# Kernel tuning notes

Measured on AMD Instinct MI355X. Metric: run time of the kernel, lower is better.

The kernel has to match this reference:

```python
import jax, jax.numpy as jnp
import numpy as np

B, N, E, H, R, L, VOCAB, KINDS = 8, 4096, 524288, 128, 8, 2, 100000, 8


def setup_inputs() -> dict:
    key = jax.random.key(0)
    ks = jax.random.split(key, 12)
    concept_ids = jax.random.randint(ks[0], (B, N), 1, VOCAB)  # avoid padding_idx 0
    kind_ids = jax.random.randint(ks[1], (B, N), 0, KINDS)
    node_mask = jnp.ones((B, N), dtype=jnp.int32)
    # edges constrained within each batch block (module assumes per-subgraph edges)
    e_batch = jax.random.randint(ks[2], (E,), 0, B)
    src = e_batch * N + jax.random.randint(ks[3], (E,), 0, N)
    dst = e_batch * N + jax.random.randint(ks[4], (E,), 0, N)
    edge_index = jnp.stack([src, dst], axis=0)
    edge_type = jax.random.randint(ks[5], (E,), 0, R)
    s = 0.02
    concept_emb = jax.random.normal(ks[6], (VOCAB, H), jnp.float32) * s
    concept_emb = concept_emb.at[0].set(0.0)  # padding_idx=0
    kind_emb = jax.random.normal(ks[7], (KINDS, H), jnp.float32) * s
    proj_W = jax.random.normal(ks[8], (H, H), jnp.float32) * s
    proj_b = jnp.zeros((H,), jnp.float32)
    self_W = jax.random.normal(ks[9], (L, H, H), jnp.float32) * s
    self_b = jnp.zeros((L, H), jnp.float32)
    rel_W = jax.random.normal(ks[10], (L, R, H, H), jnp.float32) * s
    return dict(pkg_node_concept_ids=concept_ids, pkg_node_kind_ids=kind_ids,
                pkg_node_mask=node_mask, pkg_edge_index=edge_index,
                pkg_edge_type=edge_type, concept_emb=concept_emb, kind_emb=kind_emb,
                proj_W=proj_W, proj_b=proj_b, self_W=self_W, self_b=self_b, rel_W=rel_W)


def reference(pkg_node_concept_ids, pkg_node_kind_ids, pkg_node_mask,
              pkg_edge_index, pkg_edge_type, concept_emb, kind_emb,
              proj_W, proj_b, self_W, self_b, rel_W):
    b, n = pkg_node_concept_ids.shape
    num_nodes = b * n
    # input embedding + projection (dropout = identity in eval)
    x = concept_emb[pkg_node_concept_ids] + kind_emb[pkg_node_kind_ids]  # [B,N,H]
    x = jnp.einsum('bnh,gh->bng', x, proj_W) + proj_b
    x = x.reshape(num_nodes, -1)  # packed node states [B*N, H]
    src, dst = pkg_edge_index[0], pkg_edge_index[1]
    deg = jax.ops.segment_sum(jnp.ones_like(src, dtype=x.dtype), dst,
                              num_segments=num_nodes)[:, None]
    deg = jnp.maximum(deg, 1.0)
    n_layers, n_rel = rel_W.shape[0], rel_W.shape[1]
    for l in range(n_layers):
        xs = x[src]  # [E,H] gather
        msgs = jnp.zeros_like(xs)
        for r in range(n_rel):
            msgs = msgs + jnp.where((pkg_edge_type == r)[:, None],
                                    xs @ rel_W[l, r].T, 0.0)
        agg = jax.ops.segment_sum(msgs, dst, num_segments=num_nodes) / deg
        x = jax.nn.relu(x @ self_W[l].T + self_b[l] + agg)
    out = x.reshape(b, n, -1) * pkg_node_mask[..., None].astype(x.dtype)
    return out
```

## Files before the change

kernel.cpp:

```cpp
#include <hip/hip_runtime.h>
#include <hip/hip_bf16.h>

#define NODES 32768
#define HD 128
#define NE 524288
#define NR 8

typedef unsigned int u32;
typedef unsigned short u16;
typedef __attribute__((ext_vector_type(8))) short bf16x8;
typedef __attribute__((ext_vector_type(4))) float f32x4;

#define XH_OFF   (0u)
#define XL_OFF   (8u<<20)
#define Y_OFF    (16u<<20)
#define Z_OFF    (80u<<20)
#define ADJ_OFF  (96u<<20)
#define RP_OFF   (98u<<20)
#define CUR_OFF  ((98u<<20)+(256u<<10))
#define BSUM_OFF ((98u<<20)+(512u<<10))
#define BP_OFF   ((98u<<20)+(640u<<10))

#define BP_LAYER 294912

__device__ __forceinline__ float bflo(u32 u){ union{u32 i;float f;}c; c.i=u<<16; return c.f; }
__device__ __forceinline__ float bfhi(u32 u){ union{u32 i;float f;}c; c.i=u&0xffff0000u; return c.f; }
__device__ __forceinline__ u16 f2bf(float f){
  u32 u=__float_as_uint(f);
  u32 r=u + 0x7fffu + ((u>>16)&1u);
  return (u16)(r>>16);
}
__device__ __forceinline__ float bf2f(u16 h){ return __uint_as_float(((u32)h)<<16); }

__device__ __forceinline__ void gl_lds16(const void* g, void* l){
  __builtin_amdgcn_global_load_lds((const __attribute__((address_space(1))) u32*)g,
                                   (__attribute__((address_space(3))) u32*)l, 16, 0, 0);
}

__device__ __forceinline__ void fma64(const float* At, const float* Wt,
                                      int mq, int gq, float acc[8][4])
{
#pragma unroll 8
  for(int kk=0;kk<64;kk++){
    const float4 a0=*(const float4*)&At[kk*68+mq*8];
    const float4 a1=*(const float4*)&At[kk*68+mq*8+4];
    const float4 w =*(const float4*)&Wt[kk*132+gq*4];
    float av[8]={a0.x,a0.y,a0.z,a0.w,a1.x,a1.y,a1.z,a1.w};
#pragma unroll
    for(int i=0;i<8;i++){
      acc[i][0]=fmaf(av[i],w.x,acc[i][0]);
      acc[i][1]=fmaf(av[i],w.y,acc[i][1]);
      acc[i][2]=fmaf(av[i],w.z,acc[i][2]);
      acc[i][3]=fmaf(av[i],w.w,acc[i][3]);
    }
  }
}

__global__ __launch_bounds__(256) void embed_gemm(
    const int* __restrict__ cid, const int* __restrict__ kid,
    const float* __restrict__ cemb, const float* __restrict__ kemb,
    const float* __restrict__ pW, const float* __restrict__ pb,
    u16* __restrict__ xh, u16* __restrict__ xl)
{
  __shared__ float At[64*68];
  __shared__ float Wt[64*132];
  const int tid=threadIdx.x;
  const int d0=blockIdx.x*64;
  const int mq=tid>>5, gq=tid&31;
  float acc[8][4];
#pragma unroll
  for(int i=0;i<8;i++){ acc[i][0]=0.f; acc[i][1]=0.f; acc[i][2]=0.f; acc[i][3]=0.f; }

  for(int c=0;c<2;c++){
    const int h0=c*64;
    __syncthreads();
    { int m=tid>>2; int hh=(tid&3)*16;
      int ci=cid[d0+m], ki=kid[d0+m];
      const float* cp=cemb+(size_t)ci*HD+h0+hh;
      const float* kp=kemb+(size_t)ki*HD+h0+hh;
      float* ap=&At[hh*68+m];
#pragma unroll
      for(int j=0;j<16;j+=4){
        float4 a=*(const float4*)(cp+j);
        float4 b=*(const float4*)(kp+j);
        ap[(j+0)*68]=a.x+b.x; ap[(j+1)*68]=a.y+b.y;
        ap[(j+2)*68]=a.z+b.z; ap[(j+3)*68]=a.w+b.w;
      }
    }
    { int g=tid>>1; int hh=(tid&1)*32;
      const float* wp=pW+(size_t)g*HD+h0+hh;
      float* wl=&Wt[hh*132+g];
#pragma unroll
      for(int j=0;j<32;j+=4){
        float4 w=*(const float4*)(wp+j);
        wl[(j+0)*132]=w.x; wl[(j+1)*132]=w.y; wl[(j+2)*132]=w.z; wl[(j+3)*132]=w.w;
      }
    }
    __syncthreads();
    fma64(At,Wt,mq,gq,acc);
  }
  const float4 bias=*(const float4*)&pb[gq*4];
#pragma unroll
  for(int i=0;i<8;i++){
    int m=d0+mq*8+i;
    float v[4]={acc[i][0]+bias.x,acc[i][1]+bias.y,acc[i][2]+bias.z,acc[i][3]+bias.w};
    u16 hb[4], lb[4];
#pragma unroll
    for(int j=0;j<4;j++){ hb[j]=f2bf(v[j]); lb[j]=f2bf(v[j]-bf2f(hb[j])); }
    uint2 hv={(u32)hb[0]|((u32)hb[1]<<16),(u32)hb[2]|((u32)hb[3]<<16)};
    uint2 lv={(u32)lb[0]|((u32)lb[1]<<16),(u32)lb[2]|((u32)lb[3]<<16)};
    *(uint2*)&xh[(size_t)m*HD+gq*4]=hv;
    *(uint2*)&xl[(size_t)m*HD+gq*4]=lv;
  }
}

__global__ void prep_w(const float* __restrict__ rW, const float* __restrict__ sW,
                       u16* __restrict__ Bp)
{
  int idx=blockIdx.x*256+threadIdx.x;
  int l=idx/147456;
  int rem=idx%147456;
  int t=rem>>14;
  int kn=rem&16383;
  int k=kn>>7, n=kn&127;
  float w;
  if(t<8) w=rW[(((size_t)l*NR+t)*HD+n)*HD+k];
  else    w=sW[((size_t)l*HD+n)*HD+k];
  u16* base=Bp+(size_t)l*BP_LAYER+(size_t)t*32768;
  int ks=k>>5, q=(k>>3)&3, j=k&7;
  size_t off=((size_t)ks*128+n)*32+q*8+j;
  u16 hb=f2bf(w);
  u16 lb=f2bf(w-bf2f(hb));
  base[off]=hb;
  base[off+16384]=lb;
}

__global__ void count_deg(const int* __restrict__ dst, u32* __restrict__ cnt){
  int e=blockIdx.x*256+threadIdx.x;
  atomicAdd(&cnt[dst[e]],1u);
}

__global__ void scan1(const u32* __restrict__ cnt, u32* __restrict__ rp, u32* __restrict__ bsum){
  __shared__ u32 sh[256];
  int t=threadIdx.x; int base=blockIdx.x*256;
  u32 v=cnt[base+t]; sh[t]=v; __syncthreads();
  for(int off=1;off<256;off<<=1){
    u32 tv=(t>=off)?sh[t-off]:0u; __syncthreads();
    sh[t]+=tv; __syncthreads();
  }
  rp[base+t]=sh[t]-v;
  if(t==255) bsum[blockIdx.x]=sh[255];
}

__global__ void scan2(u32* __restrict__ bsum, u32* __restrict__ rp){
  __shared__ u32 sh[128];
  int t=threadIdx.x;
  u32 v=bsum[t]; sh[t]=v; __syncthreads();
  for(int off=1;off<128;off<<=1){
    u32 tv=(t>=off)?sh[t-off]:0u; __syncthreads();
    sh[t]+=tv; __syncthreads();
  }
  bsum[t]=sh[t]-v;
  if(t==0) rp[NODES]=NE;
}

__global__ void scan3(u32* __restrict__ rp, const u32* __restrict__ bsum){
  int i=blockIdx.x*256+threadIdx.x;
  rp[i]+=bsum[blockIdx.x];
}

__global__ void scatter_edges(const int* __restrict__ src, const int* __restrict__ dst,
                              const int* __restrict__ et, const u32* __restrict__ rp,
                              u32* __restrict__ cur, u32* __restrict__ adj){
  int e=blockIdx.x*256+threadIdx.x;
  int d=dst[e];
  u32 pos=atomicAdd(&cur[d],1u);
  adj[rp[d]+pos]=(u32)src[e] | ((u32)et[e]<<16);
}

__global__ __launch_bounds__(256,3) void gemm_y(
    const u16* __restrict__ xhi, const u16* __restrict__ xlo,
    const u16* __restrict__ Bt, u16* __restrict__ y, float* __restrict__ z)
{
  __shared__ u16 Atile[128*128];
  const int tid=threadIdx.x;
  const int wave=tid>>6, lane=tid&63;
  const int wm=wave>>1, wn=wave&1;
  const int q=lane>>4;
  const int d0=blockIdx.x*128;
  const int t=blockIdx.y;
  const u16* Btile=Bt+(size_t)t*32768;

  f32x4 acc[4][4];
#pragma unroll
  for(int a=0;a<4;a++)
#pragma unroll
    for(int b=0;b<4;b++) acc[a][b]=(f32x4){0.f,0.f,0.f,0.f};

  const int st_c  = lane&15;
  const int st_rin= lane>>4;

#pragma unroll
  for(int i=0;i<8;i++){
    int rbase=wave*32+i*4;
    int r=rbase+st_rin;
    int g=st_c ^ (r&15);
    gl_lds16(xhi+(size_t)(d0+r)*HD+g*8, &Atile[rbase*128]);
  }
  __syncthreads();

#pragma unroll
  for(int ks=0;ks<4;ks++){
    bf16x8 afr[4];
#pragma unroll
    for(int tm=0;tm<4;tm++){
      int m=wm*64+tm*16+(lane&15);
      afr[tm]=*(const bf16x8*)&Atile[m*128+(((ks*4)+q)^(m&15))*8];
    }
#pragma unroll
    for(int s=0;s<2;s++){
      const u16* Bb=Btile+s*16384;
#pragma unroll
      for(int tn=0;tn<4;tn++){
        int n=wn*64+tn*16+(lane&15);
        bf16x8 bfr=*(const bf16x8*)&Bb[((size_t)ks*128+n)*32+q*8];
#pragma unroll
        for(int tm=0;tm<4;tm++)
          acc[tm][tn]=__builtin_amdgcn_mfma_f32_16x16x32_bf16(afr[tm],bfr,acc[tm][tn],0,0,0);
      }
    }
  }

  __syncthreads();
#pragma unroll
  for(int i=0;i<8;i++){
    int rbase=wave*32+i*4;
    int r=rbase+st_rin;
    int g=st_c ^ (r&15);
    gl_lds16(xlo+(size_t)(d0+r)*HD+g*8, &Atile[rbase*128]);
  }
  __syncthreads();

#pragma unroll
  for(int ks=0;ks<4;ks++){
    bf16x8 afr[4];
#pragma unroll
    for(int tm=0;tm<4;tm++){
      int m=wm*64+tm*16+(lane&15);
      afr[tm]=*(const bf16x8*)&Atile[m*128+(((ks*4)+q)^(m&15))*8];
    }
#pragma unroll
    for(int tn=0;tn<4;tn++){
      int n=wn*64+tn*16+(lane&15);
      bf16x8 bfr=*(const bf16x8*)&Btile[((size_t)ks*128+n)*32+q*8];
#pragma unroll
      for(int tm=0;tm<4;tm++)
        acc[tm][tn]=__builtin_amdgcn_mfma_f32_16x16x32_bf16(afr[tm],bfr,acc[tm][tn],0,0,0);
    }
  }

  if(t<8){
    u16* yt=y+((size_t)t*NODES+d0)*HD;
#pragma unroll
    for(int tn=0;tn<4;tn++){
      int n=wn*64+tn*16+(lane&15);
#pragma unroll
      for(int tm=0;tm<4;tm++){
        int rbase=wm*64+tm*16+q*4;
#pragma unroll
        for(int r=0;r<4;r++)
          yt[(size_t)(rbase+r)*HD+n]=f2bf(acc[tm][tn][r]);
      }
    }
  } else {
    float* zt=z+(size_t)d0*HD;
#pragma unroll
    for(int tn=0;tn<4;tn++){
      int n=wn*64+tn*16+(lane&15);
#pragma unroll
      for(int tm=0;tm<4;tm++){
        int rbase=wm*64+tm*16+q*4;
#pragma unroll
        for(int r=0;r<4;r++)
          zt[(size_t)(rbase+r)*HD+n]=acc[tm][tn][r];
      }
    }
  }
}

__global__ __launch_bounds__(256) void gather_combine(
    const u32* __restrict__ y, const float* __restrict__ z,
    const u32* __restrict__ adj, const u32* __restrict__ rp,
    const float* __restrict__ sb, const int* __restrict__ mask,
    u32* __restrict__ xh, u32* __restrict__ xl, float* __restrict__ outf, int last)
{
  const int wave=threadIdx.x>>6, lane=threadIdx.x&63;
  const int node=blockIdx.x*4+wave;
  const int beg=(int)rp[node], end=(int)rp[node+1];
  float a0=0.f, a1=0.f;
  int e=beg;
  for(; e+8<=end; e+=8){
    u32 qv[8], vv[8];
#pragma unroll
    for(int i=0;i<8;i++) qv[i]=adj[e+i];
#pragma unroll
    for(int i=0;i<8;i++) vv[i]=y[((size_t)(qv[i]>>16)*NODES+(qv[i]&0x7fffu))*64+lane];
#pragma unroll
    for(int i=0;i<8;i++){ a0+=bflo(vv[i]); a1+=bfhi(vv[i]); }
  }
  for(; e<end; ++e){
    u32 qq=adj[e];
    u32 v=y[((size_t)(qq>>16)*NODES+(qq&0x7fffu))*64+lane];
    a0+=bflo(v); a1+=bfhi(v);
  }
  float inv=1.f/fmaxf((float)(end-beg),1.f);
  float2 zz=*(const float2*)&z[(size_t)node*HD+2*lane];
  float2 bb=*(const float2*)&sb[2*lane];
  float v0=fmaxf(zz.x+a0*inv+bb.x,0.f);
  float v1=fmaxf(zz.y+a1*inv+bb.y,0.f);
  if(last){
    float mk=(float)mask[node];
    float2 o={v0*mk,v1*mk};
    *(float2*)&outf[(size_t)node*HD+2*lane]=o;
  } else {
    u16 h0=f2bf(v0), h1=f2bf(v1);
    u16 l0=f2bf(v0-bf2f(h0)), l1=f2bf(v1-bf2f(h1));
    xh[(size_t)node*64+lane]=(u32)h0|((u32)h1<<16);
    xl[(size_t)node*64+lane]=(u32)l0|((u32)l1<<16);
  }
}

extern "C" void kernel_launch(void* const* d_in, const int* in_sizes, int n_in,
                              void* d_out, int out_size, void* d_ws, size_t ws_size,
                              hipStream_t stream)
{
  (void)in_sizes; (void)n_in; (void)out_size; (void)ws_size;
  const int*   cid =(const int*)  d_in[0];
  const int*   kid =(const int*)  d_in[1];
  const int*   mask=(const int*)  d_in[2];
  const int*   ei  =(const int*)  d_in[3];
  const int*   et  =(const int*)  d_in[4];
  const float* cemb=(const float*)d_in[5];
  const float* kemb=(const float*)d_in[6];
  const float* pW  =(const float*)d_in[7];
  const float* pb  =(const float*)d_in[8];
  const float* sW  =(const float*)d_in[9];
  const float* sb  =(const float*)d_in[10];
  const float* rW  =(const float*)d_in[11];
  float* out=(float*)d_out;
  char*  ws =(char*)d_ws;

  u16* xh =(u16*)(ws+XH_OFF);
  u16* xl =(u16*)(ws+XL_OFF);
  u16* y  =(u16*)(ws+Y_OFF);
  float* z=(float*)(ws+Z_OFF);
  u32* adj =(u32*)(ws+ADJ_OFF);
  u32* rp  =(u32*)(ws+RP_OFF);
  u32* cur =(u32*)(ws+CUR_OFF);
  u32* bsum=(u32*)(ws+BSUM_OFF);
  u16* Bp  =(u16*)(ws+BP_OFF);
  const int* srcA=ei;
  const int* dstA=ei+NE;

  hipMemsetAsync(cur,0,NODES*sizeof(u32),stream);
  prep_w<<<1152,256,0,stream>>>(rW,sW,Bp);
  embed_gemm<<<NODES/64,256,0,stream>>>(cid,kid,cemb,kemb,pW,pb,xh,xl);
  count_deg<<<NE/256,256,0,stream>>>(dstA,cur);
  scan1<<<NODES/256,256,0,stream>>>(cur,rp,bsum);
  scan2<<<1,128,0,stream>>>(bsum,rp);
  scan3<<<NODES/256,256,0,stream>>>(rp,bsum);
  hipMemsetAsync(cur,0,NODES*sizeof(u32),stream);
  scatter_edges<<<NE/256,256,0,stream>>>(srcA,dstA,et,rp,cur,adj);

  gemm_y<<<dim3(NODES/128,9),256,0,stream>>>(xh,xl,Bp,y,z);
  gather_combine<<<NODES/4,256,0,stream>>>((const u32*)y,z,adj,rp,sb,mask,(u32*)xh,(u32*)xl,out,0);
  gemm_y<<<dim3(NODES/128,9),256,0,stream>>>(xh,xl,Bp+BP_LAYER,y,z);
  gather_combine<<<NODES/4,256,0,stream>>>((const u32*)y,z,adj,rp,sb+HD,mask,(u32*)xh,(u32*)xl,out,1);
}
```

Measured before the change: 343.1 us.

## Use MFMA for embedding projection, fold scan fixup, restructure gather and GEMM

Several changes land together. The FP32 FMA embedding projection becomes a split-bf16 MFMA GEMM, with the projection weight prepacked in prep_w. The scan3 kernel and the second memset go away by folding the block offsets into the consumers and clearing the counter inside scan1. gemm_y loads the hi and lo tiles together into a doubled LDS buffer at 2 blocks per CU. gather_combine now loads 64 adjacency entries per wave, broadcasts them with shuffles, and gathers two edges per wave with 8-byte loads, using a precomputed flat row index. The risks are lower occupancy in gemm_y and extra adds in the gather.

Result: faster. 312.2 us (-9.0%).

```diff
diff --git a/kernel.cpp b/kernel.cpp
--- a/kernel.cpp
+++ b/kernel.cpp
@@ -22,6 +22,7 @@
 #define BP_OFF   ((98u<<20)+(640u<<10))
 
 #define BP_LAYER 294912
+#define PP_ELEM  589824
 
 __device__ __forceinline__ float bflo(u32 u){ union{u32 i;float f;}c; c.i=u<<16; return c.f; }
 __device__ __forceinline__ float bfhi(u32 u){ union{u32 i;float f;}c; c.i=u&0xffff0000u; return c.f; }
@@ -37,102 +38,142 @@
                                    (__attribute__((address_space(3))) u32*)l, 16, 0, 0);
 }
 
-__device__ __forceinline__ void fma64(const float* At, const float* Wt,
-                                      int mq, int gq, float acc[8][4])
+__global__ void prep_w(const float* __restrict__ rW, const float* __restrict__ sW,
+                       const float* __restrict__ pWg, u16* __restrict__ Bp)
 {
-#pragma unroll 8
-  for(int kk=0;kk<64;kk++){
-    const float4 a0=*(const float4*)&At[kk*68+mq*8];
-    const float4 a1=*(const float4*)&At[kk*68+mq*8+4];
-    const float4 w =*(const float4*)&Wt[kk*132+gq*4];
-    float av[8]={a0.x,a0.y,a0.z,a0.w,a1.x,a1.y,a1.z,a1.w};
-#pragma unroll
-    for(int i=0;i<8;i++){
-      acc[i][0]=fmaf(av[i],w.x,acc[i][0]);
-      acc[i][1]=fmaf(av[i],w.y,acc[i][1]);
-      acc[i][2]=fmaf(av[i],w.z,acc[i][2]);
-      acc[i][3]=fmaf(av[i],w.w,acc[i][3]);
-    }
-  }
-}
-
-__global__ __launch_bounds__(256) void embed_gemm(
+  int idx=blockIdx.x*256+threadIdx.x;
+  if(idx<294912){
+    int l=idx/147456;
+    int rem=idx%147456;
+    int t=rem>>14;
+    int kn=rem&16383;
+    int k=kn>>7, n=kn&127;
+    float w;
+    if(t<8) w=rW[(((size_t)l*NR+t)*HD+n)*HD+k];
+    else    w=sW[((size_t)l*HD+n)*HD+k];
+    u16* base=Bp+(size_t)l*BP_LAYER+(size_t)t*32768;
+    int ks=k>>5, q=(k>>3)&3, j=k&7;
+    size_t off=((size_t)ks*128+n)*32+q*8+j;
+    u16 hb=f2bf(w);
+    u16 lb=f2bf(w-bf2f(hb));
+    base[off]=hb;
+    base[off+16384]=lb;
+  } else {
+    int kn=idx-294912;
+    int k=kn>>7, n=kn&127;
+    float w=pWg[(size_t)n*HD+k];
+    u16* base=Bp+PP_ELEM;
+    int ks=k>>5, q=(k>>3)&3, j=k&7;
+    size_t off=((size_t)ks*128+n)*32+q*8+j;
+    u16 hb=f2bf(w);
+    u16 lb=f2bf(w-bf2f(hb));
+    base[off]=hb;
+    base[off+16384]=lb;
+  }
+}
+
+__global__ __launch_bounds__(256,2) void embed_mfma(
     const int* __restrict__ cid, const int* __restrict__ kid,
     const float* __restrict__ cemb, const float* __restrict__ kemb,
-    const float* __restrict__ pW, const float* __restrict__ pb,
+    const u16* __restrict__ PP, const float* __restrict__ pb,
     u16* __restrict__ xh, u16* __restrict__ xl)
 {
-  __shared__ float At[64*68];
-  __shared__ float Wt[64*132];
+  __shared__ u16 Atile[2][128*128];
   const int tid=threadIdx.x;
-  const int d0=blockIdx.x*64;
-  const int mq=tid>>5, gq=tid&31;
-  float acc[8][4];
-#pragma unroll
-  for(int i=0;i<8;i++){ acc[i][0]=0.f; acc[i][1]=0.f; acc[i][2]=0.f; acc[i][3]=0.f; }
-
-  for(int c=0;c<2;c++){
-    const int h0=c*64;
-    __syncthreads();
-    { int m=tid>>2; int hh=(tid&3)*16;
-      int ci=cid[d0+m], ki=kid[d0+m];
-      const float* cp=cemb+(size_t)ci*HD+h0+hh;
-      const float* kp=kemb+(size_t)ki*HD+h0+hh;
-      float* ap=&At[hh*68+m];
-#pragma unroll
-      for(int j=0;j<16;j+=4){
-        float4 a=*(const float4*)(cp+j);
-        float4 b=*(const float4*)(kp+j);
-        ap[(j+0)*68]=a.x+b.x; ap[(j+1)*68]=a.y+b.y;
-        ap[(j+2)*68]=a.z+b.z; ap[(j+3)*68]=a.w+b.w;
-      }
-    }
-    { int g=tid>>1; int hh=(tid&1)*32;
-      const float* wp=pW+(size_t)g*HD+h0+hh;
-      float* wl=&Wt[hh*132+g];
-#pragma unroll
-      for(int j=0;j<32;j+=4){
-        float4 w=*(const float4*)(wp+j);
-        wl[(j+0)*132]=w.x; wl[(j+1)*132]=w.y; wl[(j+2)*132]=w.z; wl[(j+3)*132]=w.w;
-      }
-    }
-    __syncthreads();
-    fma64(At,Wt,mq,gq,acc);
-  }
-  const float4 bias=*(const float4*)&pb[gq*4];
-#pragma unroll
-  for(int i=0;i<8;i++){
-    int m=d0+mq*8+i;
-    float v[4]={acc[i][0]+bias.x,acc[i][1]+bias.y,acc[i][2]+bias.z,acc[i][3]+bias.w};
-    u16 hb[4], lb[4];
-#pragma unroll
-    for(int j=0;j<4;j++){ hb[j]=f2bf(v[j]); lb[j]=f2bf(v[j]-bf2f(hb[j])); }
-    uint2 hv={(u32)hb[0]|((u32)hb[1]<<16),(u32)hb[2]|((u32)hb[3]<<16)};
-    uint2 lv={(u32)lb[0]|((u32)lb[1]<<16),(u32)lb[2]|((u32)lb[3]<<16)};
-    *(uint2*)&xh[(size_t)m*HD+gq*4]=hv;
-    *(uint2*)&xl[(size_t)m*HD+gq*4]=lv;
-  }
-}
-
-__global__ void prep_w(const float* __restrict__ rW, const float* __restrict__ sW,
-                       u16* __restrict__ Bp)
-{
-  int idx=blockIdx.x*256+threadIdx.x;
-  int l=idx/147456;
-  int rem=idx%147456;
-  int t=rem>>14;
-  int kn=rem&16383;
-  int k=kn>>7, n=kn&127;
-  float w;
-  if(t<8) w=rW[(((size_t)l*NR+t)*HD+n)*HD+k];
-  else    w=sW[((size_t)l*HD+n)*HD+k];
-  u16* base=Bp+(size_t)l*BP_LAYER+(size_t)t*32768;
-  int ks=k>>5, q=(k>>3)&3, j=k&7;
-  size_t off=((size_t)ks*128+n)*32+q*8+j;
-  u16 hb=f2bf(w);
-  u16 lb=f2bf(w-bf2f(hb));
-  base[off]=hb;
-  base[off+16384]=lb;
+  const int wave=tid>>6, lane=tid&63;
+  const int wm=wave>>1, wn=wave&1;
+  const int q=lane>>4;
+  const int d0=blockIdx.x*128;
+
+  { int r=tid>>1, half=tid&1;
+    int ci=cid[d0+r], ki=kid[d0+r];
+    const float* cp=cemb+(size_t)ci*HD+half*64;
+    const float* kp=kemb+(size_t)ki*HD+half*64;
+#pragma unroll
+    for(int cc=0;cc<8;cc++){
+      float4 a0=*(const float4*)(cp+cc*8);
+      float4 a1=*(const float4*)(cp+cc*8+4);
+      float4 b0=*(const float4*)(kp+cc*8);
+      float4 b1=*(const float4*)(kp+cc*8+4);
+      float v[8]={a0.x+b0.x,a0.y+b0.y,a0.z+b0.z,a0.w+b0.w,
+                  a1.x+b1.x,a1.y+b1.y,a1.z+b1.z,a1.w+b1.w};
+      u16 hb[8], lb[8];
+#pragma unroll
+      for(int j=0;j<8;j++){ hb[j]=f2bf(v[j]); lb[j]=f2bf(v[j]-bf2f(hb[j])); }
+      int chunk=half*8+cc;
+      int dst=r*128+(chunk^(r&15))*8;
+      uint4 hv={(u32)hb[0]|((u32)hb[1]<<16),(u32)hb[2]|((u32)hb[3]<<16),
+                (u32)hb[4]|((u32)hb[5]<<16),(u32)hb[6]|((u32)hb[7]<<16)};
+      uint4 lv={(u32)lb[0]|((u32)lb[1]<<16),(u32)lb[2]|((u32)lb[3]<<16),
+                (u32)lb[4]|((u32)lb[5]<<16),(u32)lb[6]|((u32)lb[7]<<16)};
+      *(uint4*)&Atile[0][dst]=hv;
+      *(uint4*)&Atile[1][dst]=lv;
+    }
+  }
+  __syncthreads();
+
+  f32x4 acc[4][4];
+#pragma unroll
+  for(int a=0;a<4;a++)
+#pragma unroll
+    for(int b=0;b<4;b++) acc[a][b]=(f32x4){0.f,0.f,0.f,0.f};
+
+#pragma unroll
+  for(int ks=0;ks<4;ks++){
+    bf16x8 ah[4];
+#pragma unroll
+    for(int tm=0;tm<4;tm++){
+      int m=wm*64+tm*16+(lane&15);
+      ah[tm]=*(const bf16x8*)&Atile[0][m*128+(((ks*4)+q)^(m&15))*8];
+    }
+#pragma unroll
+    for(int s=0;s<2;s++){
+      const u16* Bb=PP+s*16384;
+#pragma unroll
+      for(int tn=0;tn<4;tn++){
+        int n=wn*64+tn*16+(lane&15);
+        bf16x8 bfr=*(const bf16x8*)&Bb[((size_t)ks*128+n)*32+q*8];
+#pragma unroll
+        for(int tm=0;tm<4;tm++)
+          acc[tm][tn]=__builtin_amdgcn_mfma_f32_16x16x32_bf16(ah[tm],bfr,acc[tm][tn],0,0,0);
+      }
+    }
+  }
+#pragma unroll
+  for(int ks=0;ks<4;ks++){
+    bf16x8 al[4];
+#pragma unroll
+    for(int tm=0;tm<4;tm++){
+      int m=wm*64+tm*16+(lane&15);
+      al[tm]=*(const bf16x8*)&Atile[1][m*128+(((ks*4)+q)^(m&15))*8];
+    }
+#pragma unroll
+    for(int tn=0;tn<4;tn++){
+      int n=wn*64+tn*16+(lane&15);
+      bf16x8 bfr=*(const bf16x8*)&PP[((size_t)ks*128+n)*32+q*8];
+#pragma unroll
+      for(int tm=0;tm<4;tm++)
+        acc[tm][tn]=__builtin_amdgcn_mfma_f32_16x16x32_bf16(al[tm],bfr,acc[tm][tn],0,0,0);
+    }
+  }
+
+#pragma unroll
+  for(int tn=0;tn<4;tn++){
+    int n=wn*64+tn*16+(lane&15);
+    float b=pb[n];
+#pragma unroll
+    for(int tm=0;tm<4;tm++){
+      int rbase=d0+wm*64+tm*16+q*4;
+#pragma unroll
+      for(int r=0;r<4;r++){
+        float v=acc[tm][tn][r]+b;
+        u16 hb=f2bf(v);
+        u16 lb=f2bf(v-bf2f(hb));
+        xh[(size_t)(rbase+r)*HD+n]=hb;
+        xl[(size_t)(rbase+r)*HD+n]=lb;
+      }
+    }
+  }
 }
 
 __global__ void count_deg(const int* __restrict__ dst, u32* __restrict__ cnt){
@@ -140,10 +181,12 @@
   atomicAdd(&cnt[dst[e]],1u);
 }
 
-__global__ void scan1(const u32* __restrict__ cnt, u32* __restrict__ rp, u32* __restrict__ bsum){
+__global__ void scan1(u32* __restrict__ cnt, u32* __restrict__ rp, u32* __restrict__ bsum){
   __shared__ u32 sh[256];
   int t=threadIdx.x; int base=blockIdx.x*256;
-  u32 v=cnt[base+t]; sh[t]=v; __syncthreads();
+  u32 v=cnt[base+t]; sh[t]=v;
+  cnt[base+t]=0u;
+  __syncthreads();
   for(int off=1;off<256;off<<=1){
     u32 tv=(t>=off)?sh[t-off]:0u; __syncthreads();
     sh[t]+=tv; __syncthreads();
@@ -161,28 +204,24 @@
     sh[t]+=tv; __syncthreads();
   }
   bsum[t]=sh[t]-v;
-  if(t==0) rp[NODES]=NE;
-}
-
-__global__ void scan3(u32* __restrict__ rp, const u32* __restrict__ bsum){
-  int i=blockIdx.x*256+threadIdx.x;
-  rp[i]+=bsum[blockIdx.x];
+  if(t==0){ rp[NODES]=NE; bsum[128]=0u; }
 }
 
 __global__ void scatter_edges(const int* __restrict__ src, const int* __restrict__ dst,
                               const int* __restrict__ et, const u32* __restrict__ rp,
+                              const u32* __restrict__ bsum,
                               u32* __restrict__ cur, u32* __restrict__ adj){
   int e=blockIdx.x*256+threadIdx.x;
   int d=dst[e];
   u32 pos=atomicAdd(&cur[d],1u);
-  adj[rp[d]+pos]=(u32)src[e] | ((u32)et[e]<<16);
-}
-
-__global__ __launch_bounds__(256,3) void gemm_y(
+  adj[rp[d]+bsum[d>>8]+pos]=(u32)(et[e]*NODES+src[e]);
+}
+
+__global__ __launch_bounds__(256,2) void gemm_y(
     const u16* __restrict__ xhi, const u16* __restrict__ xlo,
     const u16* __restrict__ Bt, u16* __restrict__ y, float* __restrict__ z)
 {
-  __shared__ u16 Atile[128*128];
+  __shared__ u16 Atile[2][128*128];
   const int tid=threadIdx.x;
   const int wave=tid>>6, lane=tid&63;
   const int wm=wave>>1, wn=wave&1;
@@ -191,12 +230,6 @@
   const int t=blockIdx.y;
   const u16* Btile=Bt+(size_t)t*32768;
 
-  f32x4 acc[4][4];
-#pragma unroll
-  for(int a=0;a<4;a++)
-#pragma unroll
-    for(int b=0;b<4;b++) acc[a][b]=(f32x4){0.f,0.f,0.f,0.f};
-
   const int st_c  = lane&15;
   const int st_rin= lane>>4;
 
@@ -205,49 +238,51 @@
     int rbase=wave*32+i*4;
     int r=rbase+st_rin;
     int g=st_c ^ (r&15);
-    gl_lds16(xhi+(size_t)(d0+r)*HD+g*8, &Atile[rbase*128]);
-  }
-  __syncthreads();
-
-#pragma unroll
-  for(int ks=0;ks<4;ks++){
-    bf16x8 afr[4];
-#pragma unroll
-    for(int tm=0;tm<4;tm++){
-      int m=wm*64+tm*16+(lane&15);
-      afr[tm]=*(const bf16x8*)&Atile[m*128+(((ks*4)+q)^(m&15))*8];
-    }
-#pragma unroll
-    for(int s=0;s<2;s++){
-      const u16* Bb=Btile+s*16384;
-#pragma unroll
-      for(int tn=0;tn<4;tn++){
-        int n=wn*64+tn*16+(lane&15);
-        bf16x8 bfr=*(const bf16x8*)&Bb[((size_t)ks*128+n)*32+q*8];
-#pragma unroll
-        for(int tm=0;tm<4;tm++)
-          acc[tm][tn]=__builtin_amdgcn_mfma_f32_16x16x32_bf16(afr[tm],bfr,acc[tm][tn],0,0,0);
-      }
-    }
-  }
-
-  __syncthreads();
+    gl_lds16(xhi+(size_t)(d0+r)*HD+g*8, &Atile[0][rbase*128]);
+  }
 #pragma unroll
   for(int i=0;i<8;i++){
     int rbase=wave*32+i*4;
     int r=rbase+st_rin;
     int g=st_c ^ (r&15);
-    gl_lds16(xlo+(size_t)(d0+r)*HD+g*8, &Atile[rbase*128]);
+    gl_lds16(xlo+(size_t)(d0+r)*HD+g*8, &Atile[1][rbase*128]);
   }
   __syncthreads();
 
+  f32x4 acc[4][4];
+#pragma unroll
+  for(int a=0;a<4;a++)
+#pragma unroll
+    for(int b=0;b<4;b++) acc[a][b]=(f32x4){0.f,0.f,0.f,0.f};
+
 #pragma unroll
   for(int ks=0;ks<4;ks++){
-    bf16x8 afr[4];
+    bf16x8 ah[4];
 #pragma unroll
     for(int tm=0;tm<4;tm++){
       int m=wm*64+tm*16+(lane&15);
-      afr[tm]=*(const bf16x8*)&Atile[m*128+(((ks*4)+q)^(m&15))*8];
+      ah[tm]=*(const bf16x8*)&Atile[0][m*128+(((ks*4)+q)^(m&15))*8];
+    }
+#pragma unroll
+    for(int s=0;s<2;s++){
+      const u16* Bb=Btile+s*16384;
+#pragma unroll
+      for(int tn=0;tn<4;tn++){
+        int n=wn*64+tn*16+(lane&15);
+        bf16x8 bfr=*(const bf16x8*)&Bb[((size_t)ks*128+n)*32+q*8];
+#pragma unroll
+        for(int tm=0;tm<4;tm++)
+          acc[tm][tn]=__builtin_amdgcn_mfma_f32_16x16x32_bf16(ah[tm],bfr,acc[tm][tn],0,0,0);
+      }
+    }
+  }
+#pragma unroll
+  for(int ks=0;ks<4;ks++){
+    bf16x8 al[4];
+#pragma unroll
+    for(int tm=0;tm<4;tm++){
+      int m=wm*64+tm*16+(lane&15);
+      al[tm]=*(const bf16x8*)&Atile[1][m*128+(((ks*4)+q)^(m&15))*8];
     }
 #pragma unroll
     for(int tn=0;tn<4;tn++){
@@ -255,7 +290,7 @@
       bf16x8 bfr=*(const bf16x8*)&Btile[((size_t)ks*128+n)*32+q*8];
 #pragma unroll
       for(int tm=0;tm<4;tm++)
-        acc[tm][tn]=__builtin_amdgcn_mfma_f32_16x16x32_bf16(afr[tm],bfr,acc[tm][tn],0,0,0);
+        acc[tm][tn]=__builtin_amdgcn_mfma_f32_16x16x32_bf16(al[tm],bfr,acc[tm][tn],0,0,0);
     }
   }
 
@@ -289,44 +324,73 @@
 }
 
 __global__ __launch_bounds__(256) void gather_combine(
-    const u32* __restrict__ y, const float* __restrict__ z,
-    const u32* __restrict__ adj, const u32* __restrict__ rp,
+    const uint2* __restrict__ yy, const float* __restrict__ z,
+    const u32* __restrict__ adj, const u32* __restrict__ rp, const u32* __restrict__ bsum,
     const float* __restrict__ sb, const int* __restrict__ mask,
     u32* __restrict__ xh, u32* __restrict__ xl, float* __restrict__ outf, int last)
 {
   const int wave=threadIdx.x>>6, lane=threadIdx.x&63;
   const int node=blockIdx.x*4+wave;
-  const int beg=(int)rp[node], end=(int)rp[node+1];
-  float a0=0.f, a1=0.f;
-  int e=beg;
-  for(; e+8<=end; e+=8){
-    u32 qv[8], vv[8];
-#pragma unroll
-    for(int i=0;i<8;i++) qv[i]=adj[e+i];
-#pragma unroll
-    for(int i=0;i<8;i++) vv[i]=y[((size_t)(qv[i]>>16)*NODES+(qv[i]&0x7fffu))*64+lane];
-#pragma unroll
-    for(int i=0;i<8;i++){ a0+=bflo(vv[i]); a1+=bfhi(vv[i]); }
-  }
-  for(; e<end; ++e){
-    u32 qq=adj[e];
-    u32 v=y[((size_t)(qq>>16)*NODES+(qq&0x7fffu))*64+lane];
-    a0+=bflo(v); a1+=bfhi(v);
-  }
-  float inv=1.f/fmaxf((float)(end-beg),1.f);
-  float2 zz=*(const float2*)&z[(size_t)node*HD+2*lane];
-  float2 bb=*(const float2*)&sb[2*lane];
-  float v0=fmaxf(zz.x+a0*inv+bb.x,0.f);
-  float v1=fmaxf(zz.y+a1*inv+bb.y,0.f);
-  if(last){
-    float mk=(float)mask[node];
-    float2 o={v0*mk,v1*mk};
-    *(float2*)&outf[(size_t)node*HD+2*lane]=o;
-  } else {
-    u16 h0=f2bf(v0), h1=f2bf(v1);
-    u16 l0=f2bf(v0-bf2f(h0)), l1=f2bf(v1-bf2f(h1));
-    xh[(size_t)node*64+lane]=(u32)h0|((u32)h1<<16);
-    xl[(size_t)node*64+lane]=(u32)l0|((u32)l1<<16);
+  const int sub=lane>>5, c=lane&31;
+  const int beg=(int)(rp[node]+bsum[node>>8]);
+  const int end=(int)(rp[node+1]+bsum[(node+1)>>8]);
+  float a0=0.f,a1=0.f,a2=0.f,a3=0.f;
+
+  for(int base=beg; base<end; base+=64){
+    int nk=end-base; if(nk>64) nk=64;
+    u32 adjv = (lane<nk) ? adj[base+lane] : 0u;
+    int i=0;
+    for(; i+16<=nk; i+=16){
+      uint2 vv[8];
+#pragma unroll
+      for(int j=0;j<8;j++){
+        u32 row=(u32)__shfl((int)adjv, i+j*2+sub);
+        vv[j]=yy[(size_t)row*32+c];
+      }
+#pragma unroll
+      for(int j=0;j<8;j++){
+        a0+=bflo(vv[j].x); a1+=bfhi(vv[j].x);
+        a2+=bflo(vv[j].y); a3+=bfhi(vv[j].y);
+      }
+    }
+    for(; i+2<=nk; i+=2){
+      u32 row=(u32)__shfl((int)adjv, i+sub);
+      uint2 v=yy[(size_t)row*32+c];
+      a0+=bflo(v.x); a1+=bfhi(v.x); a2+=bflo(v.y); a3+=bfhi(v.y);
+    }
+    if(i<nk){
+      u32 row=(u32)__shfl((int)adjv, i);
+      if(sub==0){
+        uint2 v=yy[(size_t)row*32+c];
+        a0+=bflo(v.x); a1+=bfhi(v.x); a2+=bflo(v.y); a3+=bfhi(v.y);
+      }
+    }
+  }
+
+  a0+=__shfl_xor(a0,32); a1+=__shfl_xor(a1,32);
+  a2+=__shfl_xor(a2,32); a3+=__shfl_xor(a3,32);
+
+  if(sub==0){
+    float inv=1.f/fmaxf((float)(end-beg),1.f);
+    float4 zz=*(const float4*)&z[(size_t)node*HD+c*4];
+    float4 bb=*(const float4*)&sb[c*4];
+    float v0=fmaxf(zz.x+a0*inv+bb.x,0.f);
+    float v1=fmaxf(zz.y+a1*inv+bb.y,0.f);
+    float v2=fmaxf(zz.z+a2*inv+bb.z,0.f);
+    float v3=fmaxf(zz.w+a3*inv+bb.w,0.f);
+    if(last){
+      float mk=(float)mask[node];
+      float4 o={v0*mk,v1*mk,v2*mk,v3*mk};
+      *(float4*)&outf[(size_t)node*HD+c*4]=o;
+    } else {
+      u16 h0=f2bf(v0), h1=f2bf(v1), h2=f2bf(v2), h3=f2bf(v3);
+      u16 l0=f2bf(v0-bf2f(h0)), l1=f2bf(v1-bf2f(h1));
+      u16 l2=f2bf(v2-bf2f(h2)), l3=f2bf(v3-bf2f(h3));
+      uint2 hv={(u32)h0|((u32)h1<<16),(u32)h2|((u32)h3<<16)};
+      uint2 lv={(u32)l0|((u32)l1<<16),(u32)l2|((u32)l3<<16)};
+      *(uint2*)&xh[(size_t)node*64+c*2]=hv;
+      *(uint2*)&xl[(size_t)node*64+c*2]=lv;
+    }
   }
 }
 
@@ -363,17 +427,15 @@
   const int* dstA=ei+NE;
 
   hipMemsetAsync(cur,0,NODES*sizeof(u32),stream);
-  prep_w<<<1152,256,0,stream>>>(rW,sW,Bp);
-  embed_gemm<<<NODES/64,256,0,stream>>>(cid,kid,cemb,kemb,pW,pb,xh,xl);
+  prep_w<<<1216,256,0,stream>>>(rW,sW,pW,Bp);
+  embed_mfma<<<NODES/128,256,0,stream>>>(cid,kid,cemb,kemb,Bp+PP_ELEM,pb,xh,xl);
   count_deg<<<NE/256,256,0,stream>>>(dstA,cur);
   scan1<<<NODES/256,256,0,stream>>>(cur,rp,bsum);
   scan2<<<1,128,0,stream>>>(bsum,rp);
-  scan3<<<NODES/256,256,0,stream>>>(rp,bsum);
-  hipMemsetAsync(cur,0,NODES*sizeof(u32),stream);
-  scatter_edges<<<NE/256,256,0,stream>>>(srcA,dstA,et,rp,cur,adj);
+  scatter_edges<<<NE/256,256,0,stream>>>(srcA,dstA,et,rp,bsum,cur,adj);
 
   gemm_y<<<dim3(NODES/128,9),256,0,stream>>>(xh,xl,Bp,y,z);
-  gather_combine<<<NODES/4,256,0,stream>>>((const u32*)y,z,adj,rp,sb,mask,(u32*)xh,(u32*)xl,out,0);
+  gather_combine<<<NODES/4,256,0,stream>>>((const uint2*)y,z,adj,rp,bsum,sb,mask,(u32*)xh,(u32*)xl,out,0);
   gemm_y<<<dim3(NODES/128,9),256,0,stream>>>(xh,xl,Bp+BP_LAYER,y,z);
-  gather_combine<<<NODES/4,256,0,stream>>>((const u32*)y,z,adj,rp,sb+HD,mask,(u32*)xh,(u32*)xl,out,1);
-}
+  gather_combine<<<NODES/4,256,0,stream>>>((const uint2*)y,z,adj,rp,bsum,sb+HD,mask,(u32*)xh,(u32*)xl,out,1);
+}
```
